# Optimization experiments

Measured on AMD Instinct MI355X. Metric: run time of the kernel, lower is better.

## Reference

```python
import jax, jax.numpy as jnp
import numpy as np

N_NODES = 50000
N_EDGES = 800000


def setup_inputs() -> dict:
    key = jax.random.key(0)
    ks = jax.random.split(key, 8)
    return {
        "x": jax.random.normal(ks[0], (N_NODES, 256), dtype=jnp.float32),
        "adj_vals": jax.random.uniform(ks[1], (N_EDGES,), dtype=jnp.float32),
        "rows": jax.random.randint(ks[2], (N_EDGES,), 0, N_NODES, dtype=jnp.int32),
        "cols": jax.random.randint(ks[3], (N_EDGES,), 0, N_NODES, dtype=jnp.int32),
        "W1": jax.random.normal(ks[4], (256, 256), dtype=jnp.float32) * (1.0 / np.sqrt(256)),
        "b1": jnp.zeros((256,), dtype=jnp.float32),
        "W2": jax.random.normal(ks[5], (256, 256), dtype=jnp.float32) * (1.0 / np.sqrt(256)),
        "b2": jnp.zeros((256,), dtype=jnp.float32),
        "W3": jax.random.normal(ks[6], (256, 128), dtype=jnp.float32) * (1.0 / np.sqrt(256)),
        "b3": jnp.zeros((128,), dtype=jnp.float32),
    }


def reference(x, adj_vals, rows, cols, W1, b1, W2, b2, W3, b3):
    n = x.shape[0]

    def spmm(h):
        # sparse adjacency matmul: out[r] += val * h[c] over all edges (r, c)
        return jax.ops.segment_sum(adj_vals[:, None] * h[cols], rows, num_segments=n)

    # GCNLayer: adj @ (x @ W) + b ; ReLU between layers (dropout p=0 => identity)
    h = jax.nn.relu(spmm(x @ W1) + b1)
    h = jax.nn.relu(spmm(h @ W2) + b2)
    return spmm(h @ W3) + b3
```

## Files before the change

### kernel.cpp

```cpp
#include <hip/hip_runtime.h>
#include <hip/hip_fp16.h>


#define N_NODES 50000
#define N_EDGES 800000
#define KDIM 256
#define BK 32
#define ELLCAP 64
#define ELLB 391
#define XCB 3125
#define TRB 640

typedef __attribute__((ext_vector_type(8))) short short8;
typedef __attribute__((ext_vector_type(4))) float f32x4;

__device__ __forceinline__ ushort f2bf(float f) {
    union { float f; unsigned u; } x; x.f = f;
    unsigned r = x.u + 0x7fffu + ((x.u >> 16) & 1u);
    return (ushort)(r >> 16);
}
__device__ __forceinline__ float bf2f(ushort u) {
    union { unsigned u; float f; } x; x.u = ((unsigned)u) << 16;
    return x.f;
}

__device__ __forceinline__ void gld_lds16(const void* g, void* l) {
    __builtin_amdgcn_global_load_lds(
        (const __attribute__((address_space(1))) void*)g,
        (__attribute__((address_space(3))) void*)l, 16, 0, 0);
}

__global__ __launch_bounds__(256) void prep_kernel(
        const float* __restrict__ W1, const float* __restrict__ W2,
        const float* __restrict__ W3, ushort* __restrict__ Wt1,
        ushort* __restrict__ Wt2, ushort* __restrict__ Wt3,
        const int* __restrict__ rows, const int* __restrict__ cols,
        const float* __restrict__ vals, int* __restrict__ cnt,
        unsigned* __restrict__ cvp, const float* __restrict__ x,
        ushort* __restrict__ bufX) {
    int b = blockIdx.x;
    if (b < ELLB) {
        int e0 = (b * 256 + threadIdx.x) * 8;
        if (e0 < N_EDGES) {
            int4 ra = *(const int4*)&rows[e0];
            int4 rb = *(const int4*)&rows[e0 + 4];
            int4 ca = *(const int4*)&cols[e0];
            int4 cb = *(const int4*)&cols[e0 + 4];
            float4 va = *(const float4*)&vals[e0];
            float4 vb = *(const float4*)&vals[e0 + 4];
            int   r[8] = {ra.x, ra.y, ra.z, ra.w, rb.x, rb.y, rb.z, rb.w};
            int   c[8] = {ca.x, ca.y, ca.z, ca.w, cb.x, cb.y, cb.z, cb.w};
            float v[8] = {va.x, va.y, va.z, va.w, vb.x, vb.y, vb.z, vb.w};
            #pragma unroll
            for (int u = 0; u < 8; u++) {
                int p = atomicAdd(&cnt[r[u]], 1);
                unsigned pk = ((unsigned)c[u] << 16) |
                              (unsigned)__half_as_ushort(__float2half_rn(v[u]));
                cvp[(r[u] << 6) + p] = pk;
            }
        }
    } else if (b < ELLB + XCB) {
        int base = ((b - ELLB) * 256 + threadIdx.x) * 16;
        float4 f0 = *(const float4*)&x[base];
        float4 f1 = *(const float4*)&x[base + 4];
        float4 f2 = *(const float4*)&x[base + 8];
        float4 f3 = *(const float4*)&x[base + 12];
        short8 o0, o1;
        o0[0] = (short)f2bf(f0.x); o0[1] = (short)f2bf(f0.y);
        o0[2] = (short)f2bf(f0.z); o0[3] = (short)f2bf(f0.w);
        o0[4] = (short)f2bf(f1.x); o0[5] = (short)f2bf(f1.y);
        o0[6] = (short)f2bf(f1.z); o0[7] = (short)f2bf(f1.w);
        o1[0] = (short)f2bf(f2.x); o1[1] = (short)f2bf(f2.y);
        o1[2] = (short)f2bf(f2.z); o1[3] = (short)f2bf(f2.w);
        o1[4] = (short)f2bf(f3.x); o1[5] = (short)f2bf(f3.y);
        o1[6] = (short)f2bf(f3.z); o1[7] = (short)f2bf(f3.w);
        *(short8*)&bufX[base] = o0;
        *(short8*)&bufX[base + 8] = o1;
    } else {
        int id = (b - ELLB - XCB) * 256 + threadIdx.x;
        if (id < 65536) {
            int n = id >> 8, k = id & 255;
            Wt1[n * 256 + k] = f2bf(W1[k * 256 + n]);
        } else if (id < 131072) {
            int i = id - 65536, n = i >> 8, k = i & 255;
            Wt2[n * 256 + k] = f2bf(W2[k * 256 + n]);
        } else {
            int i = id - 131072, n = i >> 8, k = i & 255;
            Wt3[n * 256 + k] = f2bf(W3[k * 128 + n]);
        }
    }
}


template <int N>
__global__ __launch_bounds__(N, 4) void gemm_rows_kernel(
        const ushort* __restrict__ A, const ushort* __restrict__ Wt,
        ushort* __restrict__ C, int M) {
    __shared__ char smem[8192 + 2 * N * 64];

    int t = threadIdx.x;
    int lane = t & 63;
    int w = t >> 6;
    int row0 = blockIdx.x * 64;
    int wn = w * 64;
    int q = lane >> 4, mi = lane & 15;

    auto stageA = [&](int bi, int k0) {
        char* dst = smem + bi * 4096;
        #pragma unroll
        for (int i = 0; i < 256 / N; i++) {
            int g = i * N + t;
            int row = row0 + ((g >> 6) << 4) + (g & 15);
            if (row >= M) row = M - 1;
            const ushort* src = A + (size_t)row * KDIM + k0 + (((g & 63) >> 4) << 3);
            gld_lds16(src, dst + (i * N + w * 64) * 16);
        }
    };
    auto stageB = [&](int bi, int k0) {
        char* dst = smem + 8192 + bi * (N * 64);
        #pragma unroll
        for (int i = 0; i < 4; i++) {
            int g = i * N + t;
            int col = ((g >> 6) << 4) + (g & 15);
            const ushort* src = Wt + (size_t)col * KDIM + k0 + (((g & 63) >> 4) << 3);
            gld_lds16(src, dst + (i * N + w * 64) * 16);
        }
    };

    f32x4 acc[4][4];
    #pragma unroll
    for (int i = 0; i < 4; i++)
        #pragma unroll
        for (int j = 0; j < 4; j++) acc[i][j] = (f32x4)0.f;

    stageA(0, 0);
    stageB(0, 0);
    __syncthreads();

    #pragma unroll
    for (int kt = 0; kt < 8; kt++) {
        int cur = kt & 1;
        if (kt < 7) {
            stageA(cur ^ 1, (kt + 1) * BK);
            stageB(cur ^ 1, (kt + 1) * BK);
        }
        char* Ac = smem + cur * 4096;
        char* Bc = smem + 8192 + cur * (N * 64);

        short8 af[4], bfr[4];
        #pragma unroll
        for (int mt = 0; mt < 4; mt++)
            af[mt] = *(const short8*)(Ac + (mt * 64 + lane) * 16);
        #pragma unroll
        for (int nt = 0; nt < 4; nt++)
            bfr[nt] = *(const short8*)(Bc + ((w * 4 + nt) * 64 + lane) * 16);

        #pragma unroll
        for (int mt = 0; mt < 4; mt++)
            #pragma unroll
            for (int nt = 0; nt < 4; nt++)
                acc[mt][nt] = __builtin_amdgcn_mfma_f32_16x16x32_bf16(
                    af[mt], bfr[nt], acc[mt][nt], 0, 0, 0);

        __syncthreads();
    }

    ushort* Cs = (ushort*)smem;
    #pragma unroll
    for (int mt = 0; mt < 4; mt++)
        #pragma unroll
        for (int r = 0; r < 4; r++)
            #pragma unroll
            for (int nt = 0; nt < 4; nt++)
                Cs[(mt * 16 + q * 4 + r) * N + wn + nt * 16 + mi] =
                    f2bf(acc[mt][nt][r]);
    __syncthreads();
    constexpr int C8 = N / 8;
    #pragma unroll
    for (int i = 0; i < 8; i++) {
        int idx = i * N + t;
        int rr = idx / C8, gc = idx % C8;
        int grow = row0 + rr;
        if (grow < M)
            *(short8*)&C[(size_t)grow * N + gc * 8] =
                *(const short8*)&Cs[rr * N + gc * 8];
    }
}


template <int F, bool RELU, bool OUT_BF16>
__global__ __launch_bounds__(256) void spmm_kernel(
        const ushort* __restrict__ H, const int* __restrict__ cnt,
        const unsigned* __restrict__ cvp, const float* __restrict__ bias,
        void* __restrict__ out, int nrows) {
    constexpr int FL = F / 8;
    constexpr int EP = 64 / FL;
    constexpr int STEP = EP * 8;
    int wave = threadIdx.x >> 6, lane = threadIdx.x & 63;
    int r = blockIdx.x * 4 + wave;
    if (r >= nrows) return;
    int fl = lane % FL, ep = lane / FL;
    const ushort* Hl = H + fl * 8;

    float acc[8];
    #pragma unroll
    for (int j = 0; j < 8; j++) acc[j] = 0.f;

    int start = r << 6;
    int end = start + cnt[r];
    for (int base = start; base < end; base += STEP) {
        int e0 = base + ep * 8;
        uint4 ma = *(const uint4*)&cvp[e0];
        uint4 mb = *(const uint4*)&cvp[e0 + 4];
        unsigned mw[8] = {ma.x, ma.y, ma.z, ma.w, mb.x, mb.y, mb.z, mb.w};
        int   c[8];
        float v[8];
        #pragma unroll
        for (int u = 0; u < 8; u++) {
            bool ok = (e0 + u < end);
            c[u] = ok ? (int)(mw[u] >> 16) : 0;
            v[u] = ok ? __half2float(__ushort_as_half((ushort)mw[u])) : 0.f;
        }
        short8 h[8];
        #pragma unroll
        for (int u = 0; u < 8; u++)
            h[u] = *(const short8*)&Hl[(size_t)c[u] * F];
        #pragma unroll
        for (int j = 0; j < 8; j++) {
            #pragma unroll
            for (int u = 0; u < 8; u++)
                acc[j] += v[u] * bf2f((ushort)h[u][j]);
        }
    }

    #pragma unroll
    for (int off = FL; off < 64; off <<= 1)
        #pragma unroll
        for (int j = 0; j < 8; j++) acc[j] += __shfl_down(acc[j], off, 64);

    if (ep == 0) {
        #pragma unroll
        for (int j = 0; j < 8; j++) {
            float o = acc[j] + bias[fl * 8 + j];
            if (RELU) o = fmaxf(o, 0.f);
            acc[j] = o;
        }
        if (OUT_BF16) {
            short8 ob;
            #pragma unroll
            for (int j = 0; j < 8; j++) ob[j] = (short)f2bf(acc[j]);
            *(short8*)((ushort*)out + (size_t)r * F + fl * 8) = ob;
        } else {
            float* of = (float*)out + (size_t)r * F + fl * 8;
            *(float4*)&of[0] = make_float4(acc[0], acc[1], acc[2], acc[3]);
            *(float4*)&of[4] = make_float4(acc[4], acc[5], acc[6], acc[7]);
        }
    }
}


extern "C" void kernel_launch(void* const* d_in, const int* in_sizes, int n_in,
                              void* d_out, int out_size, void* d_ws, size_t ws_size,
                              hipStream_t stream) {
    const float* x    = (const float*)d_in[0];
    const float* av   = (const float*)d_in[1];
    const int*   rows = (const int*)d_in[2];
    const int*   cols = (const int*)d_in[3];
    const float* W1   = (const float*)d_in[4];
    const float* b1   = (const float*)d_in[5];
    const float* W2   = (const float*)d_in[6];
    const float* b2   = (const float*)d_in[7];
    const float* W3   = (const float*)d_in[8];
    const float* b3   = (const float*)d_in[9];
    float* out = (float*)d_out;

    const int N = N_NODES;

    char* p = (char*)d_ws;
    auto carve = [&](size_t bytes) {
        void* q = (void*)p;
        p += (bytes + 255) & ~(size_t)255;
        return q;
    };
    ushort*   bufG = (ushort*)carve((size_t)N * 256 * 2);
    ushort*   bufH = (ushort*)carve((size_t)N * 256 * 2);
    ushort*   Wt1  = (ushort*)carve((size_t)256 * 256 * 2);
    ushort*   Wt2  = (ushort*)carve((size_t)256 * 256 * 2);
    ushort*   Wt3  = (ushort*)carve((size_t)128 * 256 * 2);
    int*      cnt  = (int*)carve((size_t)N * 4);
    unsigned* cvp  = (unsigned*)carve(((size_t)N * ELLCAP + 128) * 4);

    hipMemsetAsync(cnt, 0, (size_t)N * 4, stream);

    prep_kernel<<<ELLB + XCB + TRB, 256, 0, stream>>>(
        W1, W2, W3, Wt1, Wt2, Wt3, rows, cols, av, cnt, cvp, x, bufH);

    int spmm_blocks = (N + 3) / 4;
    gemm_rows_kernel<256><<<782, 256, 0, stream>>>(bufH, Wt1, bufG, N);
    spmm_kernel<256, true, true><<<spmm_blocks, 256, 0, stream>>>(bufG, cnt, cvp, b1, bufH, N);
    gemm_rows_kernel<256><<<782, 256, 0, stream>>>(bufH, Wt2, bufG, N);
    spmm_kernel<256, true, true><<<spmm_blocks, 256, 0, stream>>>(bufG, cnt, cvp, b2, bufH, N);
    gemm_rows_kernel<128><<<782, 128, 0, stream>>>(bufH, Wt3, bufG, N);
    spmm_kernel<128, false, false><<<spmm_blocks, 256, 0, stream>>>(bufG, cnt, cvp, b3, out, N);
}
```

Measured before the change: 360.2 us.

## Fuse all GCN stages into one persistent kernel with grid barriers

Replaces the memset, prep kernel and six GEMM/SpMM launches with one persistent cooperative kernel. Grid-wide atomic barriers separate the phases, and work is distributed with grid-stride loops. The layer-3 GEMM now uses a 128x128 tile with four waves instead of 64-row tiles with two waves. This removes per-launch overhead and inter-kernel gaps, but adds barrier cost and caps occupancy at three blocks per CU for every phase. It also relies on all blocks being co-resident, which carries deadlock risk.

```diff
diff --git a/kernel.cpp b/kernel.cpp
--- a/kernel.cpp
+++ b/kernel.cpp
@@ -7,9 +7,6 @@
 #define KDIM 256
 #define BK 32
 #define ELLCAP 64
-#define ELLB 391
-#define XCB 3125
-#define TRB 640
 
 typedef __attribute__((ext_vector_type(8))) short short8;
 typedef __attribute__((ext_vector_type(4))) float f32x4;
@@ -30,54 +27,311 @@
         (__attribute__((address_space(3))) void*)l, 16, 0, 0);
 }
 
-__global__ __launch_bounds__(256) void prep_kernel(
-        const float* __restrict__ W1, const float* __restrict__ W2,
-        const float* __restrict__ W3, ushort* __restrict__ Wt1,
+__device__ __forceinline__ void gsync(unsigned* bar) {
+    __syncthreads();
+    if (threadIdx.x == 0) {
+        __threadfence();
+        unsigned nb = gridDim.x;
+        unsigned g = __hip_atomic_load(&bar[1], __ATOMIC_RELAXED,
+                                       __HIP_MEMORY_SCOPE_AGENT);
+        unsigned a = __hip_atomic_fetch_add(&bar[0], 1u, __ATOMIC_ACQ_REL,
+                                            __HIP_MEMORY_SCOPE_AGENT);
+        if (a == nb - 1) {
+            __hip_atomic_store(&bar[0], 0u, __ATOMIC_RELAXED,
+                               __HIP_MEMORY_SCOPE_AGENT);
+            __hip_atomic_fetch_add(&bar[1], 1u, __ATOMIC_RELEASE,
+                                   __HIP_MEMORY_SCOPE_AGENT);
+        } else {
+            while (__hip_atomic_load(&bar[1], __ATOMIC_ACQUIRE,
+                                     __HIP_MEMORY_SCOPE_AGENT) == g)
+                __builtin_amdgcn_s_sleep(2);
+        }
+        __threadfence();
+    }
+    __syncthreads();
+}
+
+__device__ void gemm256_phase(char* smem, const ushort* __restrict__ A,
+                              const ushort* __restrict__ Wt,
+                              ushort* __restrict__ C) {
+    const int M = N_NODES;
+    int t = threadIdx.x, lane = t & 63, w = t >> 6;
+    int q = lane >> 4, mi = lane & 15;
+    int wn = w * 64;
+
+    for (int tile = blockIdx.x; tile < 782; tile += gridDim.x) {
+        int row0 = tile * 64;
+
+        auto stageA = [&](int bi, int k0) {
+            char* dst = smem + bi * 4096;
+            int g = t;
+            int row = row0 + ((g >> 6) << 4) + (g & 15);
+            if (row >= M) row = M - 1;
+            const ushort* src = A + (size_t)row * KDIM + k0 + (((g & 63) >> 4) << 3);
+            gld_lds16(src, dst + (w * 64) * 16);
+        };
+        auto stageB = [&](int bi, int k0) {
+            char* dst = smem + 8192 + bi * 16384;
+            #pragma unroll
+            for (int i = 0; i < 4; i++) {
+                int g = i * 256 + t;
+                int col = ((g >> 6) << 4) + (g & 15);
+                const ushort* src = Wt + (size_t)col * KDIM + k0 + (((g & 63) >> 4) << 3);
+                gld_lds16(src, dst + (i * 256 + w * 64) * 16);
+            }
+        };
+
+        f32x4 acc[4][4];
+        #pragma unroll
+        for (int i = 0; i < 4; i++)
+            #pragma unroll
+            for (int j = 0; j < 4; j++) acc[i][j] = (f32x4)0.f;
+
+        stageA(0, 0);
+        stageB(0, 0);
+        __syncthreads();
+
+        #pragma unroll
+        for (int kt = 0; kt < 8; kt++) {
+            int cur = kt & 1;
+            if (kt < 7) {
+                stageA(cur ^ 1, (kt + 1) * BK);
+                stageB(cur ^ 1, (kt + 1) * BK);
+            }
+            const char* Ac = smem + cur * 4096;
+            const char* Bc = smem + 8192 + cur * 16384;
+
+            short8 af[4], bfr[4];
+            #pragma unroll
+            for (int mt = 0; mt < 4; mt++)
+                af[mt] = *(const short8*)(Ac + (mt * 64 + lane) * 16);
+            #pragma unroll
+            for (int nt = 0; nt < 4; nt++)
+                bfr[nt] = *(const short8*)(Bc + ((w * 4 + nt) * 64 + lane) * 16);
+
+            #pragma unroll
+            for (int mt = 0; mt < 4; mt++)
+                #pragma unroll
+                for (int nt = 0; nt < 4; nt++)
+                    acc[mt][nt] = __builtin_amdgcn_mfma_f32_16x16x32_bf16(
+                        af[mt], bfr[nt], acc[mt][nt], 0, 0, 0);
+
+            __syncthreads();
+        }
+
+        ushort* Cs = (ushort*)smem;
+        #pragma unroll
+        for (int mt = 0; mt < 4; mt++)
+            #pragma unroll
+            for (int r = 0; r < 4; r++)
+                #pragma unroll
+                for (int nt = 0; nt < 4; nt++)
+                    Cs[(mt * 16 + q * 4 + r) * 256 + wn + nt * 16 + mi] =
+                        f2bf(acc[mt][nt][r]);
+        __syncthreads();
+        #pragma unroll
+        for (int i = 0; i < 8; i++) {
+            int idx = i * 256 + t;
+            int rr = idx >> 5, gc = idx & 31;
+            int grow = row0 + rr;
+            if (grow < M)
+                *(short8*)&C[(size_t)grow * 256 + gc * 8] =
+                    *(const short8*)&Cs[rr * 256 + gc * 8];
+        }
+        __syncthreads();
+    }
+}
+
+__device__ void gemm128_phase(char* smem, const ushort* __restrict__ A,
+                              const ushort* __restrict__ Wt,
+                              ushort* __restrict__ C) {
+    const int M = N_NODES, N = 128;
+    int t = threadIdx.x, lane = t & 63, w = t >> 6;
+    int wbase = w * 64;
+    int wm2 = w & 1, wn2 = w >> 1;
+    int wm = wm2 * 64, wn = wn2 * 64;
+    int q = lane >> 4, mi = lane & 15;
+
+    for (int tile = blockIdx.x; tile < 391; tile += gridDim.x) {
+        int row0 = tile * 128;
+        char* Ab0 = smem;
+        char* Ab1 = smem + 8192;
+        char* Bb0 = smem + 16384;
+        char* Bb1 = smem + 24576;
+
+        auto stageA = [&](char* dst, int k0) {
+            #pragma unroll
+            for (int i = 0; i < 2; i++) {
+                int D = i * 256 + t;
+                int f = D >> 6, lp = D & 63;
+                int row = row0 + (f >> 2) * 64 + (f & 3) * 16 + (lp & 15);
+                if (row >= M) row = M - 1;
+                const ushort* g = A + (size_t)row * KDIM + k0 + (lp >> 4) * 8;
+                gld_lds16(g, dst + (i * 256 + wbase) * 16);
+            }
+        };
+        auto stageB = [&](char* dst, int k0) {
+            #pragma unroll
+            for (int i = 0; i < 2; i++) {
+                int D = i * 256 + t;
+                int f = D >> 6, lp = D & 63;
+                int col = (f >> 2) * 64 + (f & 3) * 16 + (lp & 15);
+                const ushort* g = Wt + (size_t)col * KDIM + k0 + (lp >> 4) * 8;
+                gld_lds16(g, dst + (i * 256 + wbase) * 16);
+            }
+        };
+
+        f32x4 acc[4][4];
+        #pragma unroll
+        for (int i = 0; i < 4; i++)
+            #pragma unroll
+            for (int j = 0; j < 4; j++) acc[i][j] = (f32x4)0.f;
+
+        stageA(Ab0, 0);
+        stageB(Bb0, 0);
+        __syncthreads();
+
+        #pragma unroll
+        for (int kt = 0; kt < 8; kt++) {
+            char* Acur = (kt & 1) ? Ab1 : Ab0;
+            char* Bcur = (kt & 1) ? Bb1 : Bb0;
+            if (kt < 7) {
+                stageA((kt & 1) ? Ab0 : Ab1, (kt + 1) * BK);
+                stageB((kt & 1) ? Bb0 : Bb1, (kt + 1) * BK);
+            }
+            short8 af[4], bfr[4];
+            #pragma unroll
+            for (int mt = 0; mt < 4; mt++)
+                af[mt] = *(const short8*)(Acur + ((wm2 * 4 + mt) * 64 + lane) * 16);
+            #pragma unroll
+            for (int nt = 0; nt < 4; nt++)
+                bfr[nt] = *(const short8*)(Bcur + ((wn2 * 4 + nt) * 64 + lane) * 16);
+
+            #pragma unroll
+            for (int mt = 0; mt < 4; mt++)
+                #pragma unroll
+                for (int nt = 0; nt < 4; nt++)
+                    acc[mt][nt] = __builtin_amdgcn_mfma_f32_16x16x32_bf16(
+                        af[mt], bfr[nt], acc[mt][nt], 0, 0, 0);
+
+            __syncthreads();
+        }
+
+        ushort* Cs = (ushort*)smem;
+        #pragma unroll
+        for (int mt = 0; mt < 4; mt++)
+            #pragma unroll
+            for (int r = 0; r < 4; r++)
+                #pragma unroll
+                for (int nt = 0; nt < 4; nt++)
+                    Cs[(wm + mt * 16 + q * 4 + r) * N + wn + nt * 16 + mi] =
+                        f2bf(acc[mt][nt][r]);
+        __syncthreads();
+        #pragma unroll
+        for (int i = 0; i < 8; i++) {
+            int idx = i * 256 + t;
+            int rr = idx >> 4, gc = idx & 15;
+            int grow = row0 + rr;
+            if (grow < M)
+                *(short8*)&C[(size_t)grow * N + gc * 8] =
+                    *(const short8*)&Cs[rr * N + gc * 8];
+        }
+        __syncthreads();
+    }
+}
+
+template <int F, bool RELU, bool OUT_BF16>
+__device__ void spmm_phase(const ushort* __restrict__ H,
+                           const int* __restrict__ cnt,
+                           const unsigned* __restrict__ cvp,
+                           const float* __restrict__ bias,
+                           void* __restrict__ out) {
+    constexpr int FL = F / 8;
+    constexpr int EP = 64 / FL;
+    constexpr int STEP = EP * 8;
+    int wave = threadIdx.x >> 6, lane = threadIdx.x & 63;
+    int fl = lane % FL, ep = lane / FL;
+    const ushort* Hl = H + fl * 8;
+
+    for (int rb = blockIdx.x; rb < 12500; rb += gridDim.x) {
+        int r = rb * 4 + wave;
+
+        float acc[8];
+        #pragma unroll
+        for (int j = 0; j < 8; j++) acc[j] = 0.f;
+
+        int start = r << 6;
+        int end = start + cnt[r];
+        for (int base = start; base < end; base += STEP) {
+            int e0 = base + ep * 8;
+            uint4 ma = *(const uint4*)&cvp[e0];
+            uint4 mb = *(const uint4*)&cvp[e0 + 4];
+            unsigned mw[8] = {ma.x, ma.y, ma.z, ma.w, mb.x, mb.y, mb.z, mb.w};
+            int   c[8];
+            float v[8];
+            #pragma unroll
+            for (int u = 0; u < 8; u++) {
+                bool ok = (e0 + u < end);
+                c[u] = ok ? (int)(mw[u] >> 16) : 0;
+                v[u] = ok ? __half2float(__ushort_as_half((ushort)mw[u])) : 0.f;
+            }
+            short8 h[8];
+            #pragma unroll
+            for (int u = 0; u < 8; u++)
+                h[u] = *(const short8*)&Hl[(size_t)c[u] * F];
+            #pragma unroll
+            for (int j = 0; j < 8; j++) {
+                #pragma unroll
+                for (int u = 0; u < 8; u++)
+                    acc[j] += v[u] * bf2f((ushort)h[u][j]);
+            }
+        }
+
+        #pragma unroll
+        for (int off = FL; off < 64; off <<= 1)
+            #pragma unroll
+            for (int j = 0; j < 8; j++) acc[j] += __shfl_down(acc[j], off, 64);
+
+        if (ep == 0) {
+            #pragma unroll
+            for (int j = 0; j < 8; j++) {
+                float o = acc[j] + bias[fl * 8 + j];
+                if (RELU) o = fmaxf(o, 0.f);
+                acc[j] = o;
+            }
+            if (OUT_BF16) {
+                short8 ob;
+                #pragma unroll
+                for (int j = 0; j < 8; j++) ob[j] = (short)f2bf(acc[j]);
+                *(short8*)((ushort*)out + (size_t)r * F + fl * 8) = ob;
+            } else {
+                float* of = (float*)out + (size_t)r * F + fl * 8;
+                *(float4*)&of[0] = make_float4(acc[0], acc[1], acc[2], acc[3]);
+                *(float4*)&of[4] = make_float4(acc[4], acc[5], acc[6], acc[7]);
+            }
+        }
+    }
+}
+
+__global__ __launch_bounds__(256, 3) void fused_gcn(
+        const float* __restrict__ x, const float* __restrict__ vals,
+        const int* __restrict__ rows, const int* __restrict__ cols,
+        const float* __restrict__ W1, const float* __restrict__ b1,
+        const float* __restrict__ W2, const float* __restrict__ b2,
+        const float* __restrict__ W3, const float* __restrict__ b3,
+        float* __restrict__ out, ushort* __restrict__ bufG,
+        ushort* __restrict__ bufH, ushort* __restrict__ Wt1,
         ushort* __restrict__ Wt2, ushort* __restrict__ Wt3,
-        const int* __restrict__ rows, const int* __restrict__ cols,
-        const float* __restrict__ vals, int* __restrict__ cnt,
-        unsigned* __restrict__ cvp, const float* __restrict__ x,
-        ushort* __restrict__ bufX) {
-    int b = blockIdx.x;
-    if (b < ELLB) {
-        int e0 = (b * 256 + threadIdx.x) * 8;
-        if (e0 < N_EDGES) {
-            int4 ra = *(const int4*)&rows[e0];
-            int4 rb = *(const int4*)&rows[e0 + 4];
-            int4 ca = *(const int4*)&cols[e0];
-            int4 cb = *(const int4*)&cols[e0 + 4];
-            float4 va = *(const float4*)&vals[e0];
-            float4 vb = *(const float4*)&vals[e0 + 4];
-            int   r[8] = {ra.x, ra.y, ra.z, ra.w, rb.x, rb.y, rb.z, rb.w};
-            int   c[8] = {ca.x, ca.y, ca.z, ca.w, cb.x, cb.y, cb.z, cb.w};
-            float v[8] = {va.x, va.y, va.z, va.w, vb.x, vb.y, vb.z, vb.w};
-            #pragma unroll
-            for (int u = 0; u < 8; u++) {
-                int p = atomicAdd(&cnt[r[u]], 1);
-                unsigned pk = ((unsigned)c[u] << 16) |
-                              (unsigned)__half_as_ushort(__float2half_rn(v[u]));
-                cvp[(r[u] << 6) + p] = pk;
-            }
-        }
-    } else if (b < ELLB + XCB) {
-        int base = ((b - ELLB) * 256 + threadIdx.x) * 16;
-        float4 f0 = *(const float4*)&x[base];
-        float4 f1 = *(const float4*)&x[base + 4];
-        float4 f2 = *(const float4*)&x[base + 8];
-        float4 f3 = *(const float4*)&x[base + 12];
-        short8 o0, o1;
-        o0[0] = (short)f2bf(f0.x); o0[1] = (short)f2bf(f0.y);
-        o0[2] = (short)f2bf(f0.z); o0[3] = (short)f2bf(f0.w);
-        o0[4] = (short)f2bf(f1.x); o0[5] = (short)f2bf(f1.y);
-        o0[6] = (short)f2bf(f1.z); o0[7] = (short)f2bf(f1.w);
-        o1[0] = (short)f2bf(f2.x); o1[1] = (short)f2bf(f2.y);
-        o1[2] = (short)f2bf(f2.z); o1[3] = (short)f2bf(f2.w);
-        o1[4] = (short)f2bf(f3.x); o1[5] = (short)f2bf(f3.y);
-        o1[6] = (short)f2bf(f3.z); o1[7] = (short)f2bf(f3.w);
-        *(short8*)&bufX[base] = o0;
-        *(short8*)&bufX[base + 8] = o1;
-    } else {
-        int id = (b - ELLB - XCB) * 256 + threadIdx.x;
+        int* __restrict__ cnt, unsigned* __restrict__ cvp,
+        unsigned* __restrict__ bar) {
+    __shared__ char smem[40960];
+
+    int b = blockIdx.x, t = threadIdx.x;
+    int nthr = gridDim.x << 8;
+    int gid = (b << 8) + t;
+
+    for (int id = gid; id < 50048; id += nthr) cnt[id] = 0;
+    for (int id = gid; id < 163840; id += nthr) {
         if (id < 65536) {
             int n = id >> 8, k = id & 255;
             Wt1[n * 256 + k] = f2bf(W1[k * 256 + n]);
@@ -89,173 +343,63 @@
             Wt3[n * 256 + k] = f2bf(W3[k * 128 + n]);
         }
     }
-}
-
-
-template <int N>
-__global__ __launch_bounds__(N, 4) void gemm_rows_kernel(
-        const ushort* __restrict__ A, const ushort* __restrict__ Wt,
-        ushort* __restrict__ C, int M) {
-    __shared__ char smem[8192 + 2 * N * 64];
-
-    int t = threadIdx.x;
-    int lane = t & 63;
-    int w = t >> 6;
-    int row0 = blockIdx.x * 64;
-    int wn = w * 64;
-    int q = lane >> 4, mi = lane & 15;
-
-    auto stageA = [&](int bi, int k0) {
-        char* dst = smem + bi * 4096;
-        #pragma unroll
-        for (int i = 0; i < 256 / N; i++) {
-            int g = i * N + t;
-            int row = row0 + ((g >> 6) << 4) + (g & 15);
-            if (row >= M) row = M - 1;
-            const ushort* src = A + (size_t)row * KDIM + k0 + (((g & 63) >> 4) << 3);
-            gld_lds16(src, dst + (i * N + w * 64) * 16);
-        }
-    };
-    auto stageB = [&](int bi, int k0) {
-        char* dst = smem + 8192 + bi * (N * 64);
-        #pragma unroll
-        for (int i = 0; i < 4; i++) {
-            int g = i * N + t;
-            int col = ((g >> 6) << 4) + (g & 15);
-            const ushort* src = Wt + (size_t)col * KDIM + k0 + (((g & 63) >> 4) << 3);
-            gld_lds16(src, dst + (i * N + w * 64) * 16);
-        }
-    };
-
-    f32x4 acc[4][4];
-    #pragma unroll
-    for (int i = 0; i < 4; i++)
-        #pragma unroll
-        for (int j = 0; j < 4; j++) acc[i][j] = (f32x4)0.f;
-
-    stageA(0, 0);
-    stageB(0, 0);
-    __syncthreads();
-
-    #pragma unroll
-    for (int kt = 0; kt < 8; kt++) {
-        int cur = kt & 1;
-        if (kt < 7) {
-            stageA(cur ^ 1, (kt + 1) * BK);
-            stageB(cur ^ 1, (kt + 1) * BK);
-        }
-        char* Ac = smem + cur * 4096;
-        char* Bc = smem + 8192 + cur * (N * 64);
-
-        short8 af[4], bfr[4];
-        #pragma unroll
-        for (int mt = 0; mt < 4; mt++)
-            af[mt] = *(const short8*)(Ac + (mt * 64 + lane) * 16);
-        #pragma unroll
-        for (int nt = 0; nt < 4; nt++)
-            bfr[nt] = *(const short8*)(Bc + ((w * 4 + nt) * 64 + lane) * 16);
-
-        #pragma unroll
-        for (int mt = 0; mt < 4; mt++)
-            #pragma unroll
-            for (int nt = 0; nt < 4; nt++)
-                acc[mt][nt] = __builtin_amdgcn_mfma_f32_16x16x32_bf16(
-                    af[mt], bfr[nt], acc[mt][nt], 0, 0, 0);
-
-        __syncthreads();
-    }
-
-    ushort* Cs = (ushort*)smem;
-    #pragma unroll
-    for (int mt = 0; mt < 4; mt++)
-        #pragma unroll
-        for (int r = 0; r < 4; r++)
-            #pragma unroll
-            for (int nt = 0; nt < 4; nt++)
-                Cs[(mt * 16 + q * 4 + r) * N + wn + nt * 16 + mi] =
-                    f2bf(acc[mt][nt][r]);
-    __syncthreads();
-    constexpr int C8 = N / 8;
-    #pragma unroll
-    for (int i = 0; i < 8; i++) {
-        int idx = i * N + t;
-        int rr = idx / C8, gc = idx % C8;
-        int grow = row0 + rr;
-        if (grow < M)
-            *(short8*)&C[(size_t)grow * N + gc * 8] =
-                *(const short8*)&Cs[rr * N + gc * 8];
-    }
-}
-
-
-template <int F, bool RELU, bool OUT_BF16>
-__global__ __launch_bounds__(256) void spmm_kernel(
-        const ushort* __restrict__ H, const int* __restrict__ cnt,
-        const unsigned* __restrict__ cvp, const float* __restrict__ bias,
-        void* __restrict__ out, int nrows) {
-    constexpr int FL = F / 8;
-    constexpr int EP = 64 / FL;
-    constexpr int STEP = EP * 8;
-    int wave = threadIdx.x >> 6, lane = threadIdx.x & 63;
-    int r = blockIdx.x * 4 + wave;
-    if (r >= nrows) return;
-    int fl = lane % FL, ep = lane / FL;
-    const ushort* Hl = H + fl * 8;
-
-    float acc[8];
-    #pragma unroll
-    for (int j = 0; j < 8; j++) acc[j] = 0.f;
-
-    int start = r << 6;
-    int end = start + cnt[r];
-    for (int base = start; base < end; base += STEP) {
-        int e0 = base + ep * 8;
-        uint4 ma = *(const uint4*)&cvp[e0];
-        uint4 mb = *(const uint4*)&cvp[e0 + 4];
-        unsigned mw[8] = {ma.x, ma.y, ma.z, ma.w, mb.x, mb.y, mb.z, mb.w};
-        int   c[8];
-        float v[8];
-        #pragma unroll
-        for (int u = 0; u < 8; u++) {
-            bool ok = (e0 + u < end);
-            c[u] = ok ? (int)(mw[u] >> 16) : 0;
-            v[u] = ok ? __half2float(__ushort_as_half((ushort)mw[u])) : 0.f;
-        }
-        short8 h[8];
-        #pragma unroll
-        for (int u = 0; u < 8; u++)
-            h[u] = *(const short8*)&Hl[(size_t)c[u] * F];
-        #pragma unroll
-        for (int j = 0; j < 8; j++) {
-            #pragma unroll
-            for (int u = 0; u < 8; u++)
-                acc[j] += v[u] * bf2f((ushort)h[u][j]);
-        }
-    }
-
-    #pragma unroll
-    for (int off = FL; off < 64; off <<= 1)
-        #pragma unroll
-        for (int j = 0; j < 8; j++) acc[j] += __shfl_down(acc[j], off, 64);
-
-    if (ep == 0) {
-        #pragma unroll
-        for (int j = 0; j < 8; j++) {
-            float o = acc[j] + bias[fl * 8 + j];
-            if (RELU) o = fmaxf(o, 0.f);
-            acc[j] = o;
-        }
-        if (OUT_BF16) {
-            short8 ob;
-            #pragma unroll
-            for (int j = 0; j < 8; j++) ob[j] = (short)f2bf(acc[j]);
-            *(short8*)((ushort*)out + (size_t)r * F + fl * 8) = ob;
-        } else {
-            float* of = (float*)out + (size_t)r * F + fl * 8;
-            *(float4*)&of[0] = make_float4(acc[0], acc[1], acc[2], acc[3]);
-            *(float4*)&of[4] = make_float4(acc[4], acc[5], acc[6], acc[7]);
-        }
-    }
+    gsync(bar);
+
+    int EB = gridDim.x / 3;
+    if (b < EB) {
+        for (int o = gid; o < N_EDGES / 8; o += (EB << 8)) {
+            int e0 = o * 8;
+            int4 ra = *(const int4*)&rows[e0];
+            int4 rb2 = *(const int4*)&rows[e0 + 4];
+            int4 ca = *(const int4*)&cols[e0];
+            int4 cb = *(const int4*)&cols[e0 + 4];
+            float4 va = *(const float4*)&vals[e0];
+            float4 vb = *(const float4*)&vals[e0 + 4];
+            int   r[8] = {ra.x, ra.y, ra.z, ra.w, rb2.x, rb2.y, rb2.z, rb2.w};
+            int   c[8] = {ca.x, ca.y, ca.z, ca.w, cb.x, cb.y, cb.z, cb.w};
+            float v[8] = {va.x, va.y, va.z, va.w, vb.x, vb.y, vb.z, vb.w};
+            #pragma unroll
+            for (int u = 0; u < 8; u++) {
+                int p = atomicAdd(&cnt[r[u]], 1);
+                unsigned pk = ((unsigned)c[u] << 16) |
+                              (unsigned)__half_as_ushort(__float2half_rn(v[u]));
+                cvp[(r[u] << 6) + p] = pk;
+            }
+        }
+    } else {
+        int NB = gridDim.x - EB;
+        for (int g = ((b - EB) << 8) + t; g < 800000; g += (NB << 8)) {
+            int base = g * 16;
+            float4 f0 = *(const float4*)&x[base];
+            float4 f1 = *(const float4*)&x[base + 4];
+            float4 f2 = *(const float4*)&x[base + 8];
+            float4 f3 = *(const float4*)&x[base + 12];
+            short8 o0, o1;
+            o0[0] = (short)f2bf(f0.x); o0[1] = (short)f2bf(f0.y);
+            o0[2] = (short)f2bf(f0.z); o0[3] = (short)f2bf(f0.w);
+            o0[4] = (short)f2bf(f1.x); o0[5] = (short)f2bf(f1.y);
+            o0[6] = (short)f2bf(f1.z); o0[7] = (short)f2bf(f1.w);
+            o1[0] = (short)f2bf(f2.x); o1[1] = (short)f2bf(f2.y);
+            o1[2] = (short)f2bf(f2.z); o1[3] = (short)f2bf(f2.w);
+            o1[4] = (short)f2bf(f3.x); o1[5] = (short)f2bf(f3.y);
+            o1[6] = (short)f2bf(f3.z); o1[7] = (short)f2bf(f3.w);
+            *(short8*)&bufH[base] = o0;
+            *(short8*)&bufH[base + 8] = o1;
+        }
+    }
+    gsync(bar);
+
+    gemm256_phase(smem, bufH, Wt1, bufG);
+    gsync(bar);
+    spmm_phase<256, true, true>(bufG, cnt, cvp, b1, bufH);
+    gsync(bar);
+    gemm256_phase(smem, bufH, Wt2, bufG);
+    gsync(bar);
+    spmm_phase<256, true, true>(bufG, cnt, cvp, b2, bufH);
+    gsync(bar);
+    gemm128_phase(smem, bufH, Wt3, bufG);
+    gsync(bar);
+    spmm_phase<128, false, false>(bufG, cnt, cvp, b3, out);
 }
 
 
@@ -287,19 +431,24 @@
     ushort*   Wt1  = (ushort*)carve((size_t)256 * 256 * 2);
     ushort*   Wt2  = (ushort*)carve((size_t)256 * 256 * 2);
     ushort*   Wt3  = (ushort*)carve((size_t)128 * 256 * 2);
-    int*      cnt  = (int*)carve((size_t)N * 4);
+    int*      cnt  = (int*)carve((size_t)50048 * 4);
     unsigned* cvp  = (unsigned*)carve(((size_t)N * ELLCAP + 128) * 4);
-
-    hipMemsetAsync(cnt, 0, (size_t)N * 4, stream);
-
-    prep_kernel<<<ELLB + XCB + TRB, 256, 0, stream>>>(
-        W1, W2, W3, Wt1, Wt2, Wt3, rows, cols, av, cnt, cvp, x, bufH);
-
-    int spmm_blocks = (N + 3) / 4;
-    gemm_rows_kernel<256><<<782, 256, 0, stream>>>(bufH, Wt1, bufG, N);
-    spmm_kernel<256, true, true><<<spmm_blocks, 256, 0, stream>>>(bufG, cnt, cvp, b1, bufH, N);
-    gemm_rows_kernel<256><<<782, 256, 0, stream>>>(bufH, Wt2, bufG, N);
-    spmm_kernel<256, true, true><<<spmm_blocks, 256, 0, stream>>>(bufG, cnt, cvp, b2, bufH, N);
-    gemm_rows_kernel<128><<<782, 128, 0, stream>>>(bufH, Wt3, bufG, N);
-    spmm_kernel<128, false, false><<<spmm_blocks, 256, 0, stream>>>(bufG, cnt, cvp, b3, out, N);
-}
+    unsigned* bar  = (unsigned*)carve(256);
+
+    static int nblk = 0;
+    if (nblk == 0) {
+        int occ = 0;
+        if (hipOccupancyMaxActiveBlocksPerMultiprocessor(
+                &occ, (const void*)fused_gcn, 256, 0) != hipSuccess || occ < 1)
+            occ = 1;
+        long nb = (long)occ * 248;
+        if (nb > 744) nb = 744;
+        if (nb < 248) nb = 248;
+        nblk = (int)nb;
+    }
+
+    hipMemsetAsync(bar, 0, 16, stream);
+    fused_gcn<<<nblk, 256, 0, stream>>>(
+        x, av, rows, cols, W1, b1, W2, b2, W3, b3, out,
+        bufG, bufH, Wt1, Wt2, Wt3, cnt, cvp, bar);
+}
```

New measurement: 1.086 ms. +201.5%, slower.
